# Kernel optimization log

Measured on AMD Instinct MI355X. Metric: run time of the kernel, lower is better.

Reference implementation:

```python
import jax, jax.numpy as jnp
import numpy as np

B, T, C = 4, 2048, 1024
N_HEAD = 16
HEAD = C // N_HEAD  # 64


def _rope_tables(T, dim, base=10000.0):
    inv_freq = 1.0 / (base ** (jnp.arange(0, dim, 2, dtype=jnp.float32) / dim))
    t = jnp.arange(T, dtype=jnp.float32)
    freqs = jnp.einsum('i,j->ij', t, inv_freq)           # [T, dim/2]
    emb = jnp.concatenate([freqs, freqs], axis=-1)        # [T, dim]
    return jnp.cos(emb), jnp.sin(emb)                     # each [T, dim]


def _rotate_half(x):
    x1, x2 = x[..., : x.shape[-1] // 2], x[..., x.shape[-1] // 2:]
    return jnp.concatenate([-x2, x1], axis=-1)


def setup_inputs() -> dict:
    key = jax.random.key(0)
    ks = jax.random.split(key, 4)
    x = jax.random.normal(ks[0], (B, T, C), dtype=jnp.float32)
    w_attn = jax.random.normal(ks[1], (C, 3 * C), dtype=jnp.float32) * (1.0 / np.sqrt(C))
    b_attn = jnp.zeros((3 * C,), dtype=jnp.float32)
    w_proj = jax.random.normal(ks[2], (C, C), dtype=jnp.float32) * (1.0 / np.sqrt(C))
    b_proj = jnp.zeros((C,), dtype=jnp.float32)
    return {"x": x, "w_attn": w_attn, "b_attn": b_attn, "w_proj": w_proj, "b_proj": b_proj}


def reference(x, w_attn, b_attn, w_proj, b_proj):
    Bx, Tx, Cx = x.shape
    qkv = x @ w_attn + b_attn                             # [B,T,3C]
    q, k, v = jnp.split(qkv, 3, axis=-1)
    # [B,T,C] -> [B,H,T,hd]
    def to_heads(t):
        return t.reshape(Bx, Tx, N_HEAD, HEAD).transpose(0, 2, 1, 3)
    q, k, v = to_heads(q), to_heads(k), to_heads(v)
    cos, sin = _rope_tables(Tx, HEAD)                     # [T,hd]
    cos = cos[None, None, :, :]
    sin = sin[None, None, :, :]
    q = q * cos + _rotate_half(q) * sin
    k = k * cos + _rotate_half(k) * sin
    scale = 1.0 / np.sqrt(HEAD)
    att = jnp.einsum('bhqd,bhkd->bhqk', q, k) * scale     # [B,H,T,T]
    causal = jnp.tril(jnp.ones((Tx, Tx), dtype=bool))
    att = jnp.where(causal[None, None], att, -jnp.inf)
    att = jax.nn.softmax(att, axis=-1)
    y = jnp.einsum('bhqk,bhkd->bhqd', att, v)             # [B,H,T,hd]
    y = y.transpose(0, 2, 1, 3).reshape(Bx, Tx, Cx)
    return y @ w_proj + b_proj
```

## Files before the change

kernel.cpp:

```cpp
#include <hip/hip_runtime.h>

#define B_  4
#define T_  2048
#define C_  1024
#define NH_ 16
#define HD_ 64
#define BT_ (B_*T_)
#define N3C (3*C_)

typedef _Float16 f16;
typedef _Float16 half8 __attribute__((ext_vector_type(8)));
typedef _Float16 half4 __attribute__((ext_vector_type(4)));
typedef float f32x4 __attribute__((ext_vector_type(4)));

__device__ __forceinline__ void gld16(const f16* g, f16* l) {
  __builtin_amdgcn_global_load_lds(
      (const __attribute__((address_space(1))) unsigned int*)g,
      (__attribute__((address_space(3))) unsigned int*)l, 16, 0, 0);
}

__global__ __launch_bounds__(256) void cvt_x(const float* __restrict__ X,
                                             f16* __restrict__ X16)
{
  const int i = blockIdx.x * 256 + threadIdx.x;
  const float4 a = ((const float4*)X)[i * 2];
  const float4 b = ((const float4*)X)[i * 2 + 1];
  half8 h;
  h[0] = (f16)a.x; h[1] = (f16)a.y; h[2] = (f16)a.z; h[3] = (f16)a.w;
  h[4] = (f16)b.x; h[5] = (f16)b.y; h[6] = (f16)b.z; h[7] = (f16)b.w;
  ((half8*)X16)[i] = h;
}

__global__ __launch_bounds__(256) void cvt_transpose(
    const float* __restrict__ W, f16* __restrict__ Wt, int K, int N)
{
  __shared__ float Ls[64][65];
  const int tid = threadIdx.x;
  const int n0 = blockIdx.x * 64, k0 = blockIdx.y * 64;
#pragma unroll
  for (int j = 0; j < 4; ++j) {
    const int idx = j * 256 + tid;
    const int r = idx >> 4, c = (idx & 15) * 4;
    const float4 w = *(const float4*)(W + (size_t)(k0 + r) * N + n0 + c);
    Ls[r][c + 0] = w.x; Ls[r][c + 1] = w.y; Ls[r][c + 2] = w.z; Ls[r][c + 3] = w.w;
  }
  __syncthreads();
#pragma unroll
  for (int j = 0; j < 2; ++j) {
    const int idx = j * 256 + tid;
    const int r = idx >> 3, c = (idx & 7) * 8;
    half8 h;
#pragma unroll
    for (int u = 0; u < 8; ++u) h[u] = (f16)Ls[c + u][r];
    *(half8*)(Wt + (size_t)(n0 + r) * K + k0 + c) = h;
  }
}

__global__ __launch_bounds__(256) void gemm_qkv(
    const f16* __restrict__ A, const f16* __restrict__ Bt,
    const float* __restrict__ bias,
    f16* __restrict__ Qo, f16* __restrict__ Ko, f16* __restrict__ Vt_g)
{
  __shared__ f16 As[128 * 64];
  __shared__ f16 Bs[128 * 64];
  const int tid  = threadIdx.x;
  const int row0 = blockIdx.y * 128;
  const int col0 = blockIdx.x * 128;
  const int wave = tid >> 6, lane = tid & 63;
  const int l = lane & 15, quad = lane >> 4;
  const int wm = wave >> 1, wn = wave & 1;
  const int sr = tid >> 3;
  const int scs = ((tid & 7) ^ (sr & 7)) * 8;
  const int lq7 = l & 7;

  f32x4 acc[4][4];
#pragma unroll
  for (int mi = 0; mi < 4; ++mi)
#pragma unroll
    for (int ni = 0; ni < 4; ++ni) acc[mi][ni] = (f32x4)0.0f;

  for (int k0 = 0; k0 < C_; k0 += 64) {
    __syncthreads();
#pragma unroll
    for (int p = 0; p < 4; ++p) {
      const int r = p * 32 + sr;
      gld16(A  + (size_t)(row0 + r) * C_ + k0 + scs, &As[p * 2048 + tid * 8]);
      gld16(Bt + (size_t)(col0 + r) * C_ + k0 + scs, &Bs[p * 2048 + tid * 8]);
    }
    __syncthreads();

#pragma unroll
    for (int s = 0; s < 2; ++s) {
      half8 af[4], bf[4];
#pragma unroll
      for (int mi = 0; mi < 4; ++mi)
        af[mi] = *(const half8*)&As[(wm * 64 + mi * 16 + l) * 64 + ((((s << 2) | quad) ^ lq7) << 3)];
#pragma unroll
      for (int ni = 0; ni < 4; ++ni)
        bf[ni] = *(const half8*)&Bs[(wn * 64 + ni * 16 + l) * 64 + ((((s << 2) | quad) ^ lq7) << 3)];
#pragma unroll
      for (int mi = 0; mi < 4; ++mi)
#pragma unroll
        for (int ni = 0; ni < 4; ++ni)
          acc[mi][ni] = __builtin_amdgcn_mfma_f32_16x16x32_f16(af[mi], bf[ni], acc[mi][ni], 0, 0, 0);
    }
  }

  const int region = col0 >> 10;
  const int colw = col0 + wn * 64;
  const int h = (colw & 1023) >> 6;
  if (region < 2) {
    f16* dst = (region == 0) ? Qo : Ko;
    float invf[2];
#pragma unroll
    for (int ni = 0; ni < 2; ++ni) {
      const float fr = (float)(ni * 16 + l);
      invf[ni] = expf(-(2.0f * fr / 64.0f) * 9.210340371976184f);
    }
#pragma unroll
    for (int mi = 0; mi < 4; ++mi) {
#pragma unroll
      for (int r = 0; r < 4; ++r) {
        const int gm = row0 + wm * 64 + mi * 16 + quad * 4 + r;
        const int b = gm >> 11, t = gm & (T_ - 1);
        const size_t base = ((size_t)(b * NH_ + h) * T_ + t) * HD_;
#pragma unroll
        for (int ni = 0; ni < 2; ++ni) {
          const int d = ni * 16 + l;
          const float x1 = acc[mi][ni][r]     + bias[colw + d];
          const float x2 = acc[mi][ni + 2][r] + bias[colw + d + 32];
          float sn, cn;
          sincosf((float)t * invf[ni], &sn, &cn);
          dst[base + d]      = (f16)(x1 * cn - x2 * sn);
          dst[base + d + 32] = (f16)(x2 * cn + x1 * sn);
        }
      }
    }
  } else {
#pragma unroll
    for (int mi = 0; mi < 4; ++mi) {
      const int t0 = row0 + wm * 64 + mi * 16 + quad * 4;
      const int b = t0 >> 11, t = t0 & (T_ - 1);
#pragma unroll
      for (int ni = 0; ni < 4; ++ni) {
        const int d = ni * 16 + l;
        const float bs = bias[colw + d];
        half4 o;
#pragma unroll
        for (int r = 0; r < 4; ++r) o[r] = (f16)(acc[mi][ni][r] + bs);
        *(half4*)(Vt_g + ((size_t)((b * NH_ + h) * HD_ + d)) * T_ + t) = o;
      }
    }
  }
}

__global__ __launch_bounds__(256) void attn_mfma(
    const f16* __restrict__ Qg, const f16* __restrict__ Kg,
    const f16* __restrict__ Vt_g, f16* __restrict__ Y)
{
  __shared__ f16 Ks[64 * 64];
  __shared__ f16 Vt[64 * 64];
  const int tid  = threadIdx.x;
  const int qt   = 31 - (blockIdx.x >> 6);
  const int bh   = blockIdx.x & 63;
  const int b    = bh >> 4, h = bh & 15;
  const int wave = tid >> 6, lane = tid & 63;
  const int l    = lane & 15, quad = lane >> 4;
  const int qrow = qt * 64 + wave * 16 + l;

  const f16* qp = Qg + ((size_t)bh * T_ + qrow) * HD_;
  half8 qf[2];
#pragma unroll
  for (int s = 0; s < 2; ++s)
    qf[s] = *(const half8*)(qp + s * 32 + quad * 8);

  f32x4 O[4];
#pragma unroll
  for (int mi = 0; mi < 4; ++mi) O[mi] = (f32x4)0.0f;
  float m_run = -1e30f, l_run = 0.f;

  const f16* kbase  = Kg   + (size_t)bh * T_ * HD_;
  const f16* vtbase = Vt_g + (size_t)bh * HD_ * T_;
  const int lq7 = l & 7;

  for (int kt = 0; kt <= qt; ++kt) {
    __syncthreads();
#pragma unroll
    for (int i = 0; i < 2; ++i) {
      const int r = i * 32 + (tid >> 3);
      const int c = tid & 7;
      const int cs = ((c ^ (r & 7)) << 3);
      const half8 hk = *(const half8*)(kbase + (size_t)(kt * 64 + r) * HD_ + c * 8);
      *(half8*)&Ks[r * 64 + cs] = hk;
      const half8 hv = *(const half8*)(vtbase + (size_t)r * T_ + kt * 64 + c * 8);
      *(half8*)&Vt[r * 64 + cs] = hv;
    }
    __syncthreads();

    f32x4 St[4];
#pragma unroll
    for (int st = 0; st < 4; ++st) {
      f32x4 s_acc = (f32x4)0.0f;
#pragma unroll
      for (int s = 0; s < 2; ++s) {
        const int row = st * 16 + l;
        const half8 af = *(const half8*)&Ks[row * 64 + ((((s << 2) | quad) ^ lq7) << 3)];
        s_acc = __builtin_amdgcn_mfma_f32_16x16x32_f16(af, qf[s], s_acc, 0, 0, 0);
      }
      St[st] = s_acc;
    }

    float p[4][4];
    float cmax = -1e30f;
    const bool diag = (kt == qt);
#pragma unroll
    for (int st = 0; st < 4; ++st)
#pragma unroll
      for (int r = 0; r < 4; ++r) {
        float x = St[st][r] * 0.125f;
        if (diag) {
          const int key = kt * 64 + st * 16 + quad * 4 + r;
          if (key > qrow) x = -1e9f;
        }
        p[st][r] = x;
        cmax = fmaxf(cmax, x);
      }
    cmax = fmaxf(cmax, __shfl_xor(cmax, 16));
    cmax = fmaxf(cmax, __shfl_xor(cmax, 32));
    const float mnew  = fmaxf(m_run, cmax);
    const float alpha = __expf(m_run - mnew);
    float psum = 0.f;
#pragma unroll
    for (int st = 0; st < 4; ++st)
#pragma unroll
      for (int r = 0; r < 4; ++r) {
        const float ev = __expf(p[st][r] - mnew);
        p[st][r] = ev;
        psum += ev;
      }
    psum += __shfl_xor(psum, 16);
    psum += __shfl_xor(psum, 32);
    l_run = l_run * alpha + psum;
    m_run = mnew;

    half4 pf[4];
#pragma unroll
    for (int st = 0; st < 4; ++st) {
      pf[st][0] = (f16)p[st][0]; pf[st][1] = (f16)p[st][1];
      pf[st][2] = (f16)p[st][2]; pf[st][3] = (f16)p[st][3];
      O[st] *= alpha;
    }

#pragma unroll
    for (int mi = 0; mi < 4; ++mi) {
      const int row = mi * 16 + l;
#pragma unroll
      for (int ki = 0; ki < 4; ++ki) {
        const int kch = (ki << 1) | (quad >> 1);
        const half4 vf = *(const half4*)&Vt[row * 64 + ((kch ^ lq7) << 3) + ((quad & 1) << 2)];
        O[mi] = __builtin_amdgcn_mfma_f32_16x16x16f16(vf, pf[ki], O[mi], 0, 0, 0);
      }
    }
  }

  const float inv = 1.0f / l_run;
  f16* yp = Y + ((size_t)(b * T_) + qrow) * C_ + h * 64;
#pragma unroll
  for (int mi = 0; mi < 4; ++mi) {
    half4 o;
    o[0] = (f16)(O[mi][0] * inv); o[1] = (f16)(O[mi][1] * inv);
    o[2] = (f16)(O[mi][2] * inv); o[3] = (f16)(O[mi][3] * inv);
    *(half4*)(yp + mi * 16 + quad * 4) = o;
  }
}

__global__ __launch_bounds__(256) void gemm_proj(
    const f16* __restrict__ A, const f16* __restrict__ Bt,
    const float* __restrict__ bias, float* __restrict__ Out)
{
  __shared__ f16 As[128 * 64];
  __shared__ f16 Bs[128 * 64];
  const int tid  = threadIdx.x;
  const int row0 = blockIdx.y * 128;
  const int col0 = blockIdx.x * 128;
  const int wave = tid >> 6, lane = tid & 63;
  const int l = lane & 15, quad = lane >> 4;
  const int wm = wave >> 1, wn = wave & 1;
  const int sr = tid >> 3;
  const int scs = ((tid & 7) ^ (sr & 7)) * 8;
  const int lq7 = l & 7;

  f32x4 acc[4][4];
#pragma unroll
  for (int mi = 0; mi < 4; ++mi)
#pragma unroll
    for (int ni = 0; ni < 4; ++ni) acc[mi][ni] = (f32x4)0.0f;

  for (int k0 = 0; k0 < C_; k0 += 64) {
    __syncthreads();
#pragma unroll
    for (int p = 0; p < 4; ++p) {
      const int r = p * 32 + sr;
      gld16(A  + (size_t)(row0 + r) * C_ + k0 + scs, &As[p * 2048 + tid * 8]);
      gld16(Bt + (size_t)(col0 + r) * C_ + k0 + scs, &Bs[p * 2048 + tid * 8]);
    }
    __syncthreads();

#pragma unroll
    for (int s = 0; s < 2; ++s) {
      half8 af[4], bf[4];
#pragma unroll
      for (int mi = 0; mi < 4; ++mi)
        af[mi] = *(const half8*)&As[(wm * 64 + mi * 16 + l) * 64 + ((((s << 2) | quad) ^ lq7) << 3)];
#pragma unroll
      for (int ni = 0; ni < 4; ++ni)
        bf[ni] = *(const half8*)&Bs[(wn * 64 + ni * 16 + l) * 64 + ((((s << 2) | quad) ^ lq7) << 3)];
#pragma unroll
      for (int mi = 0; mi < 4; ++mi)
#pragma unroll
        for (int ni = 0; ni < 4; ++ni)
          acc[mi][ni] = __builtin_amdgcn_mfma_f32_16x16x32_f16(af[mi], bf[ni], acc[mi][ni], 0, 0, 0);
    }
  }

#pragma unroll
  for (int mi = 0; mi < 4; ++mi) {
#pragma unroll
    for (int ni = 0; ni < 4; ++ni) {
#pragma unroll
      for (int r = 0; r < 4; ++r) {
        const int gm = row0 + wm * 64 + mi * 16 + quad * 4 + r;
        const int n  = col0 + wn * 64 + ni * 16 + l;
        Out[(size_t)gm * C_ + n] = acc[mi][ni][r] + bias[n];
      }
    }
  }
}

extern "C" void kernel_launch(void* const* d_in, const int* in_sizes, int n_in,
                              void* d_out, int out_size, void* d_ws, size_t ws_size,
                              hipStream_t stream) {
  const float* x      = (const float*)d_in[0];
  const float* w_attn = (const float*)d_in[1];
  const float* b_attn = (const float*)d_in[2];
  const float* w_proj = (const float*)d_in[3];
  const float* b_proj = (const float*)d_in[4];
  float* out = (float*)d_out;

  const size_t elems = (size_t)BT_ * C_;
  f16* x16 = (f16*)d_ws;
  f16* wta = x16 + elems;
  f16* wtp = wta + (size_t)N3C * C_;
  f16* q   = wtp + (size_t)C_ * C_;
  f16* k   = q + elems;
  f16* vt  = k + elems;
  f16* y   = vt + elems;

  cvt_x<<<dim3(elems / 8 / 256), 256, 0, stream>>>(x, x16);
  cvt_transpose<<<dim3(N3C / 64, C_ / 64), 256, 0, stream>>>(w_attn, wta, C_, N3C);
  cvt_transpose<<<dim3(C_ / 64, C_ / 64), 256, 0, stream>>>(w_proj, wtp, C_, C_);
  gemm_qkv<<<dim3(N3C / 128, BT_ / 128), 256, 0, stream>>>(x16, wta, b_attn, q, k, vt);
  attn_mfma<<<dim3(32 * 64), 256, 0, stream>>>(q, k, vt, y);
  gemm_proj<<<dim3(C_ / 128, BT_ / 128), 256, 0, stream>>>(y, wtp, b_proj, out);
}
```

Before: 277.5 us.

## Process two query tiles per attention block and precompute RoPE cos/sin table

Each attention block now handles 128 query rows (two 64-row sets per wave), so every K/V tile staged in shared memory feeds twice as many MFMAs and global K/V traffic is halved. The grid shrinks from 2048 to 1024 blocks. A separate kernel precomputes a cos/sin table that the QKV GEMM epilogue reads instead of calling sincosf per element. The costs are more registers per thread, which can lower occupancy, fewer blocks to balance the causal workload, a wasted half tile of masked work on the diagonal, and an extra kernel launch plus table reads.

```diff
diff --git a/kernel.cpp b/kernel.cpp
--- a/kernel.cpp
+++ b/kernel.cpp
@@ -56,9 +56,19 @@
   }
 }
 
+__global__ __launch_bounds__(256) void rope_tab(float2* __restrict__ cs)
+{
+  const int i = blockIdx.x * 256 + threadIdx.x;
+  const int f = i & 31, t = i >> 5;
+  const float inv = expf(-(2.0f * (float)f / 64.0f) * 9.210340371976184f);
+  float sn, cn;
+  sincosf((float)t * inv, &sn, &cn);
+  cs[i] = make_float2(cn, sn);
+}
+
 __global__ __launch_bounds__(256) void gemm_qkv(
     const f16* __restrict__ A, const f16* __restrict__ Bt,
-    const float* __restrict__ bias,
+    const float* __restrict__ bias, const float2* __restrict__ cs,
     f16* __restrict__ Qo, f16* __restrict__ Ko, f16* __restrict__ Vt_g)
 {
   __shared__ f16 As[128 * 64];
@@ -111,12 +121,6 @@
   const int h = (colw & 1023) >> 6;
   if (region < 2) {
     f16* dst = (region == 0) ? Qo : Ko;
-    float invf[2];
-#pragma unroll
-    for (int ni = 0; ni < 2; ++ni) {
-      const float fr = (float)(ni * 16 + l);
-      invf[ni] = expf(-(2.0f * fr / 64.0f) * 9.210340371976184f);
-    }
 #pragma unroll
     for (int mi = 0; mi < 4; ++mi) {
 #pragma unroll
@@ -124,15 +128,15 @@
         const int gm = row0 + wm * 64 + mi * 16 + quad * 4 + r;
         const int b = gm >> 11, t = gm & (T_ - 1);
         const size_t base = ((size_t)(b * NH_ + h) * T_ + t) * HD_;
+        const float2* csrow = cs + t * 32;
 #pragma unroll
         for (int ni = 0; ni < 2; ++ni) {
           const int d = ni * 16 + l;
+          const float2 c2 = csrow[d];
           const float x1 = acc[mi][ni][r]     + bias[colw + d];
           const float x2 = acc[mi][ni + 2][r] + bias[colw + d + 32];
-          float sn, cn;
-          sincosf((float)t * invf[ni], &sn, &cn);
-          dst[base + d]      = (f16)(x1 * cn - x2 * sn);
-          dst[base + d + 32] = (f16)(x2 * cn + x1 * sn);
+          dst[base + d]      = (f16)(x1 * c2.x - x2 * c2.y);
+          dst[base + d + 32] = (f16)(x2 * c2.x + x1 * c2.y);
         }
       }
     }
@@ -161,94 +165,109 @@
   __shared__ f16 Ks[64 * 64];
   __shared__ f16 Vt[64 * 64];
   const int tid  = threadIdx.x;
-  const int qt   = 31 - (blockIdx.x >> 6);
+  const int qt   = 15 - (blockIdx.x >> 6);
   const int bh   = blockIdx.x & 63;
   const int b    = bh >> 4, h = bh & 15;
   const int wave = tid >> 6, lane = tid & 63;
   const int l    = lane & 15, quad = lane >> 4;
-  const int qrow = qt * 64 + wave * 16 + l;
-
-  const f16* qp = Qg + ((size_t)bh * T_ + qrow) * HD_;
-  half8 qf[2];
-#pragma unroll
-  for (int s = 0; s < 2; ++s)
-    qf[s] = *(const half8*)(qp + s * 32 + quad * 8);
-
-  f32x4 O[4];
-#pragma unroll
-  for (int mi = 0; mi < 4; ++mi) O[mi] = (f32x4)0.0f;
-  float m_run = -1e30f, l_run = 0.f;
+  const int lq7  = l & 7;
+  int qrow[2];
+  qrow[0] = qt * 128 + wave * 16 + l;
+  qrow[1] = qrow[0] + 64;
+
+  half8 qf[2][2];
+#pragma unroll
+  for (int u = 0; u < 2; ++u) {
+    const f16* qp = Qg + ((size_t)bh * T_ + qrow[u]) * HD_;
+#pragma unroll
+    for (int s = 0; s < 2; ++s)
+      qf[u][s] = *(const half8*)(qp + s * 32 + quad * 8);
+  }
+
+  f32x4 O[2][4];
+#pragma unroll
+  for (int u = 0; u < 2; ++u)
+#pragma unroll
+    for (int mi = 0; mi < 4; ++mi) O[u][mi] = (f32x4)0.0f;
+  float m_run[2] = {-1e30f, -1e30f}, l_run[2] = {0.f, 0.f};
 
   const f16* kbase  = Kg   + (size_t)bh * T_ * HD_;
   const f16* vtbase = Vt_g + (size_t)bh * HD_ * T_;
-  const int lq7 = l & 7;
-
-  for (int kt = 0; kt <= qt; ++kt) {
+
+  const int nkt = 2 * qt + 2;
+  for (int kt = 0; kt < nkt; ++kt) {
     __syncthreads();
 #pragma unroll
     for (int i = 0; i < 2; ++i) {
       const int r = i * 32 + (tid >> 3);
       const int c = tid & 7;
-      const int cs = ((c ^ (r & 7)) << 3);
+      const int cst = ((c ^ (r & 7)) << 3);
       const half8 hk = *(const half8*)(kbase + (size_t)(kt * 64 + r) * HD_ + c * 8);
-      *(half8*)&Ks[r * 64 + cs] = hk;
+      *(half8*)&Ks[r * 64 + cst] = hk;
       const half8 hv = *(const half8*)(vtbase + (size_t)r * T_ + kt * 64 + c * 8);
-      *(half8*)&Vt[r * 64 + cs] = hv;
-    }
-    __syncthreads();
-
-    f32x4 St[4];
+      *(half8*)&Vt[r * 64 + cst] = hv;
+    }
+    __syncthreads();
+
+    f32x4 St[2][4];
+#pragma unroll
+    for (int u = 0; u < 2; ++u)
+#pragma unroll
+      for (int st = 0; st < 4; ++st) St[u][st] = (f32x4)0.0f;
 #pragma unroll
     for (int st = 0; st < 4; ++st) {
-      f32x4 s_acc = (f32x4)0.0f;
 #pragma unroll
       for (int s = 0; s < 2; ++s) {
         const int row = st * 16 + l;
         const half8 af = *(const half8*)&Ks[row * 64 + ((((s << 2) | quad) ^ lq7) << 3)];
-        s_acc = __builtin_amdgcn_mfma_f32_16x16x32_f16(af, qf[s], s_acc, 0, 0, 0);
-      }
-      St[st] = s_acc;
-    }
-
-    float p[4][4];
-    float cmax = -1e30f;
-    const bool diag = (kt == qt);
-#pragma unroll
-    for (int st = 0; st < 4; ++st)
-#pragma unroll
-      for (int r = 0; r < 4; ++r) {
-        float x = St[st][r] * 0.125f;
-        if (diag) {
-          const int key = kt * 64 + st * 16 + quad * 4 + r;
-          if (key > qrow) x = -1e9f;
+#pragma unroll
+        for (int u = 0; u < 2; ++u)
+          St[u][st] = __builtin_amdgcn_mfma_f32_16x16x32_f16(af, qf[u][s], St[u][st], 0, 0, 0);
+      }
+    }
+
+    const bool domask = (kt >= 2 * qt);
+    const int k0 = kt * 64;
+    half4 pf[2][4];
+#pragma unroll
+    for (int u = 0; u < 2; ++u) {
+      float p[4][4];
+      float cmax = -1e30f;
+#pragma unroll
+      for (int st = 0; st < 4; ++st)
+#pragma unroll
+        for (int r = 0; r < 4; ++r) {
+          float x = St[u][st][r] * 0.125f;
+          if (domask) {
+            const int key = k0 + st * 16 + quad * 4 + r;
+            if (key > qrow[u]) x = -1e9f;
+          }
+          p[st][r] = x;
+          cmax = fmaxf(cmax, x);
         }
-        p[st][r] = x;
-        cmax = fmaxf(cmax, x);
-      }
-    cmax = fmaxf(cmax, __shfl_xor(cmax, 16));
-    cmax = fmaxf(cmax, __shfl_xor(cmax, 32));
-    const float mnew  = fmaxf(m_run, cmax);
-    const float alpha = __expf(m_run - mnew);
-    float psum = 0.f;
-#pragma unroll
-    for (int st = 0; st < 4; ++st)
-#pragma unroll
-      for (int r = 0; r < 4; ++r) {
-        const float ev = __expf(p[st][r] - mnew);
-        p[st][r] = ev;
-        psum += ev;
-      }
-    psum += __shfl_xor(psum, 16);
-    psum += __shfl_xor(psum, 32);
-    l_run = l_run * alpha + psum;
-    m_run = mnew;
-
-    half4 pf[4];
-#pragma unroll
-    for (int st = 0; st < 4; ++st) {
-      pf[st][0] = (f16)p[st][0]; pf[st][1] = (f16)p[st][1];
-      pf[st][2] = (f16)p[st][2]; pf[st][3] = (f16)p[st][3];
-      O[st] *= alpha;
+      cmax = fmaxf(cmax, __shfl_xor(cmax, 16));
+      cmax = fmaxf(cmax, __shfl_xor(cmax, 32));
+      const float mnew  = fmaxf(m_run[u], cmax);
+      const float alpha = __expf(m_run[u] - mnew);
+      float psum = 0.f;
+#pragma unroll
+      for (int st = 0; st < 4; ++st)
+#pragma unroll
+        for (int r = 0; r < 4; ++r) {
+          const float ev = __expf(p[st][r] - mnew);
+          p[st][r] = ev;
+          psum += ev;
+        }
+      psum += __shfl_xor(psum, 16);
+      psum += __shfl_xor(psum, 32);
+      l_run[u] = l_run[u] * alpha + psum;
+      m_run[u] = mnew;
+#pragma unroll
+      for (int st = 0; st < 4; ++st) {
+        pf[u][st][0] = (f16)p[st][0]; pf[u][st][1] = (f16)p[st][1];
+        pf[u][st][2] = (f16)p[st][2]; pf[u][st][3] = (f16)p[st][3];
+        O[u][st] *= alpha;
+      }
     }
 
 #pragma unroll
@@ -258,19 +277,24 @@
       for (int ki = 0; ki < 4; ++ki) {
         const int kch = (ki << 1) | (quad >> 1);
         const half4 vf = *(const half4*)&Vt[row * 64 + ((kch ^ lq7) << 3) + ((quad & 1) << 2)];
-        O[mi] = __builtin_amdgcn_mfma_f32_16x16x16f16(vf, pf[ki], O[mi], 0, 0, 0);
-      }
-    }
-  }
-
-  const float inv = 1.0f / l_run;
-  f16* yp = Y + ((size_t)(b * T_) + qrow) * C_ + h * 64;
-#pragma unroll
-  for (int mi = 0; mi < 4; ++mi) {
-    half4 o;
-    o[0] = (f16)(O[mi][0] * inv); o[1] = (f16)(O[mi][1] * inv);
-    o[2] = (f16)(O[mi][2] * inv); o[3] = (f16)(O[mi][3] * inv);
-    *(half4*)(yp + mi * 16 + quad * 4) = o;
+#pragma unroll
+        for (int u = 0; u < 2; ++u)
+          O[u][mi] = __builtin_amdgcn_mfma_f32_16x16x16f16(vf, pf[u][ki], O[u][mi], 0, 0, 0);
+      }
+    }
+  }
+
+#pragma unroll
+  for (int u = 0; u < 2; ++u) {
+    const float inv = 1.0f / l_run[u];
+    f16* yp = Y + ((size_t)(b * T_) + qrow[u]) * C_ + h * 64;
+#pragma unroll
+    for (int mi = 0; mi < 4; ++mi) {
+      half4 o;
+      o[0] = (f16)(O[u][mi][0] * inv); o[1] = (f16)(O[u][mi][1] * inv);
+      o[2] = (f16)(O[u][mi][2] * inv); o[3] = (f16)(O[u][mi][3] * inv);
+      *(half4*)(yp + mi * 16 + quad * 4) = o;
+    }
   }
 }
 
@@ -355,11 +379,13 @@
   f16* k   = q + elems;
   f16* vt  = k + elems;
   f16* y   = vt + elems;
-
+  float2* cs = (float2*)(y + elems);
+
+  rope_tab<<<dim3((T_ * 32) / 256), 256, 0, stream>>>(cs);
   cvt_x<<<dim3(elems / 8 / 256), 256, 0, stream>>>(x, x16);
   cvt_transpose<<<dim3(N3C / 64, C_ / 64), 256, 0, stream>>>(w_attn, wta, C_, N3C);
   cvt_transpose<<<dim3(C_ / 64, C_ / 64), 256, 0, stream>>>(w_proj, wtp, C_, C_);
-  gemm_qkv<<<dim3(N3C / 128, BT_ / 128), 256, 0, stream>>>(x16, wta, b_attn, q, k, vt);
-  attn_mfma<<<dim3(32 * 64), 256, 0, stream>>>(q, k, vt, y);
+  gemm_qkv<<<dim3(N3C / 128, BT_ / 128), 256, 0, stream>>>(x16, wta, b_attn, cs, q, k, vt);
+  attn_mfma<<<dim3(16 * 64), 256, 0, stream>>>(q, k, vt, y);
   gemm_proj<<<dim3(C_ / 128, BT_ / 128), 256, 0, stream>>>(y, wtp, b_proj, out);
 }
```

After: 284.5 us. 2.5% more time.
